# Performance work log

Hardware: AMD Instinct MI355X
Metric: run time of the kernel (lower is better)

The kernel has to match this reference:

```python
import jax, jax.numpy as jnp
import numpy as np

N, C, H, W = 64, 160, 64, 64
DIM, M = 160, 6
N_ITERS = 2
EPS_LN = 1e-5


def layer_norm(x, g, b):
    mu = jnp.mean(x, axis=-1, keepdims=True)
    var = jnp.var(x, axis=-1, keepdims=True)
    return (x - mu) * jax.lax.rsqrt(var + EPS_LN) * g + b


def setup_inputs() -> dict:
    key = jax.random.key(0)
    ks = jax.random.split(key, 10)
    d = DIM
    lin = lambda k, i, o: jax.random.normal(k, (i, o), jnp.float32) * (1.0 / np.sqrt(i))
    return {
        "feat": jax.random.normal(ks[0], (N, C, H, W), jnp.float32),
        "slots_init": jax.random.normal(ks[1], (M, d), jnp.float32) * 0.02,
        "log_tau": jnp.zeros((1,), jnp.float32),
        "kv_g": jnp.ones((C,), jnp.float32), "kv_b": jnp.zeros((C,), jnp.float32),
        "Wk": lin(ks[2], C, d), "Wv": lin(ks[3], C, d),
        "q_g": jnp.ones((d,), jnp.float32), "q_b": jnp.zeros((d,), jnp.float32),
        "Wq": lin(ks[4], d, d),
        "out_g": jnp.ones((d,), jnp.float32), "out_b": jnp.zeros((d,), jnp.float32),
        "W1": lin(ks[5], d, 2 * d), "b1": jnp.zeros((2 * d,), jnp.float32),
        "W2": lin(ks[6], 2 * d, d), "b2": jnp.zeros((d,), jnp.float32),
    }


def reference(feat, slots_init, log_tau, kv_g, kv_b, Wk, Wv, q_g, q_b, Wq,
              out_g, out_b, W1, b1, W2, b2):
    n, c, h, w = feat.shape
    scale = DIM ** (-0.5)
    # [n, l, c] tokens
    kv_in = layer_norm(feat.reshape(n, c, h * w).transpose(0, 2, 1), kv_g, kv_b)
    k = kv_in @ Wk  # [n, l, d]
    v = kv_in @ Wv  # [n, l, d]
    slots = jnp.broadcast_to(slots_init[None], (n, M, DIM))
    tau = jax.nn.softplus(log_tau) + 0.5  # [1]
    attn = None
    for _ in range(N_ITERS):
        q = layer_norm(slots, q_g, q_b) @ Wq  # [n, m, d]
        logits = jnp.einsum('nmd,nld->nml', q, k) * (scale / tau)
        attn = jax.nn.softmax(logits, axis=1)  # compete over slots
        weights = attn / jnp.clip(attn.sum(axis=-1, keepdims=True), 1e-6)
        updates = jnp.einsum('nml,nld->nmd', weights, v)
        slots = layer_norm(slots + updates, out_g, out_b)
        slots = slots + (jax.nn.gelu(slots @ W1 + b1, approximate=False) @ W2 + b2)
    attn_map = (attn / jnp.clip(attn.sum(axis=-1, keepdims=True), 1e-6)).reshape(n, M, h, w)
    return slots, attn_map
```

## Files before the change

### kernel.cpp

```cpp
#include <hip/hip_runtime.h>
#include <math.h>

#define NN 64
#define CC 160
#define LL 4096
#define DD 160
#define MM 6
#define NCH 16
#define NT 4
#define XSTR 68

#if defined(__has_builtin)
#if __has_builtin(__builtin_amdgcn_fdot2_f32_bf16)
#define HAVE_DOT2 1
#endif
#endif

__device__ __forceinline__ unsigned short f2bf(float f) {
  union { float f; unsigned int i; } v; v.f = f;
  unsigned int r = v.i + 0x7fffu + ((v.i >> 16) & 1u);
  return (unsigned short)(r >> 16);
}
__device__ __forceinline__ float u2f_lo(unsigned int w) {
  union { unsigned int i; float f; } v; v.i = w << 16; return v.f;
}
__device__ __forceinline__ float u2f_hi(unsigned int w) {
  union { unsigned int i; float f; } v; v.i = w & 0xffff0000u; return v.f;
}

#if HAVE_DOT2
typedef __bf16 v2bf __attribute__((ext_vector_type(2)));
__device__ __forceinline__ float dot2bf(unsigned int a, unsigned int b, float c) {
  union { unsigned int u; v2bf v; } ua, ub;
  ua.u = a; ub.u = b;
  return __builtin_amdgcn_fdot2_f32_bf16(ua.v, ub.v, c, false);
}
#else
__device__ __forceinline__ float dot2bf(unsigned int a, unsigned int b, float c) {
  return fmaf(u2f_hi(a), u2f_hi(b), fmaf(u2f_lo(a), u2f_lo(b), c));
}
#endif

__global__ __launch_bounds__(256) void k_trans(
    const float* __restrict__ Wv, const float* __restrict__ Wq,
    const float* __restrict__ W1, const float* __restrict__ W2,
    float* __restrict__ WvT, float* __restrict__ WqT,
    float* __restrict__ W1T, float* __restrict__ W2T) {
  int b = blockIdx.x;
  const float* src; float* dst; int R, C, tr, tc;
  if (b < 25)       { src = Wv; dst = WvT; R = 160; C = 160; int t = b;       tr = t / 5;  tc = t % 5; }
  else if (b < 50)  { src = Wq; dst = WqT; R = 160; C = 160; int t = b - 25;  tr = t / 5;  tc = t % 5; }
  else if (b < 100) { src = W1; dst = W1T; R = 160; C = 320; int t = b - 50;  tr = t / 10; tc = t % 10; }
  else              { src = W2; dst = W2T; R = 320; C = 160; int t = b - 100; tr = t / 5;  tc = t % 5; }
  __shared__ float tile[32][33];
  int r0 = tr * 32, c0 = tc * 32;
  int lr = threadIdx.x >> 5, lc = threadIdx.x & 31;
#pragma unroll
  for (int i = 0; i < 4; i++)
    tile[lr + i * 8][lc] = src[(size_t)(r0 + lr + i * 8) * C + c0 + lc];
  __syncthreads();
#pragma unroll
  for (int i = 0; i < 4; i++)
    dst[(size_t)(c0 + lr + i * 8) * R + r0 + lc] = tile[lc][lr + i * 8];
}

__global__ __launch_bounds__(512) void k_init(
    const float* log_tau, const float* slots_init, const float* q_g, const float* q_b,
    const float* Wq, const float* Wk, float* Wkq1, float* scal) {
  __shared__ float ln[MM * DD];
  __shared__ float qv[MM * DD];
  __shared__ float mu_s[MM], rs_s[MM];
  int bi = blockIdx.x, tid = threadIdx.x;
  float x = log_tau[0];
  float sp = (x > 20.f) ? x : log1pf(expf(x));
  float scv = (1.0f / sqrtf((float)DD)) / (sp + 0.5f);
  if (bi == 0 && tid == 0) scal[0] = scv;
  int w = tid >> 6, l = tid & 63;
  if (w < MM) {
    float x0 = slots_init[w * DD + l];
    float x1 = slots_init[w * DD + l + 64];
    float x2 = (l < 32) ? slots_init[w * DD + l + 128] : 0.f;
    float s = x0 + x1 + x2, ss = x0 * x0 + x1 * x1 + x2 * x2;
#pragma unroll
    for (int off = 32; off >= 1; off >>= 1) { s += __shfl_xor(s, off); ss += __shfl_xor(ss, off); }
    if (l == 0) {
      float mu = s / DD, var = ss / DD - mu * mu;
      mu_s[w] = mu; rs_s[w] = rsqrtf(var + 1e-5f);
    }
  }
  __syncthreads();
  for (int o = tid; o < MM * DD; o += 512) {
    int m = o / DD, d = o % DD;
    ln[o] = (slots_init[o] - mu_s[m]) * rs_s[m] * q_g[d] + q_b[d];
  }
  __syncthreads();
  for (int o = tid; o < MM * DD; o += 512) {
    int m = o / DD, d = o % DD;
    float acc = 0.f;
#pragma unroll 8
    for (int i = 0; i < DD; i++) acc = fmaf(ln[m * DD + i], Wq[i * DD + d], acc);
    qv[o] = acc;
  }
  __syncthreads();
  int grp = tid >> 4, l4 = tid & 15;
#pragma unroll
  for (int t = grp; t < 60; t += 32) {
    int c = bi * 10 + t / 6, m = t % 6;
    float s = 0.f;
#pragma unroll
    for (int i = 0; i < 10; i++) {
      int d = l4 + i * 16;
      s = fmaf(Wk[c * DD + d], qv[m * DD + d], s);
    }
    s += __shfl_xor(s, 1); s += __shfl_xor(s, 2);
    s += __shfl_xor(s, 4); s += __shfl_xor(s, 8);
    if (l4 == 0) Wkq1[c * 6 + m] = scv * s;
  }
}

__global__ __launch_bounds__(256) void k_init2(
    const float* Wkq1, const float* kv_g, const float* kv_b, float* P1, float* ab) {
  int tid = threadIdx.x;
  for (int o = tid; o < DD * 6; o += 256) {
    int c = o / 6;
    P1[o] = kv_g[c] * Wkq1[o];
  }
  if (tid < 192) {
    int grp = tid >> 4;
    int l = tid & 15;
    int m = grp % 6;
    const float* coef = (grp < 6) ? kv_g : kv_b;
    float s = 0.f;
#pragma unroll
    for (int i = 0; i < 10; i++) {
      int c = l + i * 16;
      s += coef[c] * Wkq1[c * 6 + m];
    }
    s += __shfl_xor(s, 1); s += __shfl_xor(s, 2);
    s += __shfl_xor(s, 4); s += __shfl_xor(s, 8);
    if (l == 0) ab[grp] = s;
  }
}

struct TileShared {
  unsigned short xb[160 * XSTR];
  float part[4][16][4][10];
  unsigned int w2_s[32][8];
  float P_s[160][8];
};

template <bool ITER2>
__device__ __forceinline__ void tile_body(
    TileShared* sh, const float* __restrict__ fb, const float* alpha, const float* beta,
    int tid, int lane, int g, int cg, int tl,
    float* Aacc, float* Sacc,
    float* __restrict__ attn_out, size_t attn_base) {
  float s4[4] = {0, 0, 0, 0}, ss4[4] = {0, 0, 0, 0};
  float lgr[6][4];
#pragma unroll
  for (int m = 0; m < 6; m++) { lgr[m][0] = 0.f; lgr[m][1] = 0.f; lgr[m][2] = 0.f; lgr[m][3] = 0.f; }
#pragma unroll
  for (int r = 0; r < 10; r++) {
    int c = g * 40 + r * 4 + cg;
    float4 xv = *(const float4*)(fb + (size_t)(r * 4) * LL);
    float4 p03 = *(const float4*)&sh->P_s[c][0];
    float2 p45 = *(const float2*)&sh->P_s[c][4];
    float xs[4] = {xv.x, xv.y, xv.z, xv.w};
#pragma unroll
    for (int j = 0; j < 4; j++) {
      float x = xs[j];
      s4[j] += x; ss4[j] = fmaf(x, x, ss4[j]);
      lgr[0][j] = fmaf(x, p03.x, lgr[0][j]); lgr[1][j] = fmaf(x, p03.y, lgr[1][j]);
      lgr[2][j] = fmaf(x, p03.z, lgr[2][j]); lgr[3][j] = fmaf(x, p03.w, lgr[3][j]);
      lgr[4][j] = fmaf(x, p45.x, lgr[4][j]); lgr[5][j] = fmaf(x, p45.y, lgr[5][j]);
    }
    uint2 pk;
    pk.x = (unsigned int)f2bf(xv.x) | ((unsigned int)f2bf(xv.y) << 16);
    pk.y = (unsigned int)f2bf(xv.z) | ((unsigned int)f2bf(xv.w) << 16);
    *(uint2*)&sh->xb[c * XSTR + 4 * tl] = pk;
  }
#pragma unroll
  for (int j = 0; j < 4; j++) {
    s4[j] += __shfl_xor(s4[j], 16);  s4[j] += __shfl_xor(s4[j], 32);
    ss4[j] += __shfl_xor(ss4[j], 16); ss4[j] += __shfl_xor(ss4[j], 32);
#pragma unroll
    for (int m = 0; m < 6; m++) {
      lgr[m][j] += __shfl_xor(lgr[m][j], 16);
      lgr[m][j] += __shfl_xor(lgr[m][j], 32);
    }
  }
  if (cg == 0) {
#pragma unroll
    for (int j = 0; j < 4; j++) {
      float* pp = &sh->part[g][tl][j][0];
      *(float2*)&pp[0] = make_float2(s4[j], ss4[j]);
      *(float2*)&pp[2] = make_float2(lgr[0][j], lgr[1][j]);
      *(float2*)&pp[4] = make_float2(lgr[2][j], lgr[3][j]);
      *(float2*)&pp[6] = make_float2(lgr[4][j], lgr[5][j]);
    }
  }
  __syncthreads();
  {
    int tg = lane >> 2, tj = lane & 3;
    float S = 0.f, SS = 0.f, L[6] = {0, 0, 0, 0, 0, 0};
#pragma unroll
    for (int g2 = 0; g2 < 4; g2++) {
      const float* pp = &sh->part[g2][tg][tj][0];
      float2 a = *(const float2*)&pp[0];
      float2 b2_ = *(const float2*)&pp[2];
      float2 c2 = *(const float2*)&pp[4];
      float2 d2 = *(const float2*)&pp[6];
      S += a.x; SS += a.y;
      L[0] += b2_.x; L[1] += b2_.y; L[2] += c2.x; L[3] += c2.y; L[4] += d2.x; L[5] += d2.y;
    }
    float mu = S * (1.0f / CC);
    float var = SS * (1.0f / CC) - mu * mu;
    float rs = rsqrtf(var + 1e-5f);
    float lg[6];
#pragma unroll
    for (int m = 0; m < 6; m++) lg[m] = rs * L[m] - rs * mu * alpha[m] + beta[m];
    float mx = lg[0];
#pragma unroll
    for (int m = 1; m < 6; m++) mx = fmaxf(mx, lg[m]);
    float e[6], sum = 0.f;
#pragma unroll
    for (int m = 0; m < 6; m++) { e[m] = __expf(lg[m] - mx); sum += e[m]; }
    float inv = 1.0f / sum;
    float att[6], wv[6];
#pragma unroll
    for (int m = 0; m < 6; m++) { att[m] = e[m] * inv; wv[m] = att[m] * rs; }
    if (g == 0) {
      float wo[6];
#pragma unroll
      for (int m = 0; m < 6; m++) wo[m] = __shfl_xor(wv[m], 1);
      if (!(lane & 1)) {
        int tp = lane >> 1;
        unsigned int pk[6];
#pragma unroll
        for (int m = 0; m < 6; m++) pk[m] = (unsigned int)f2bf(wv[m]) | ((unsigned int)f2bf(wo[m]) << 16);
        *(uint4*)&sh->w2_s[tp][0] = make_uint4(pk[0], pk[1], pk[2], pk[3]);
        *(uint2*)&sh->w2_s[tp][4] = make_uint2(pk[4], pk[5]);
      }
    } else if (g == 1) {
      if (ITER2) {
#pragma unroll
        for (int m = 0; m < 6; m++) attn_out[attn_base + lane + (size_t)m * LL] = att[m];
      }
    } else if (g == 2) {
#pragma unroll
      for (int m = 0; m < 6; m++) Sacc[m] += att[m];
    } else {
#pragma unroll
      for (int m = 0; m < 6; m++) Sacc[m] += wv[m] * mu;
    }
  }
  __syncthreads();
  if (tid < DD) {
    const unsigned short* xr = &sh->xb[tid * XSTR];
#pragma unroll
    for (int k = 0; k < 16; k++) {
      uint2 xw = *(const uint2*)(xr + 4 * k);
      uint4 wa0 = *(const uint4*)&sh->w2_s[2 * k][0];
      uint2 wb0 = *(const uint2*)&sh->w2_s[2 * k][4];
      uint4 wa1 = *(const uint4*)&sh->w2_s[2 * k + 1][0];
      uint2 wb1 = *(const uint2*)&sh->w2_s[2 * k + 1][4];
      Aacc[0] = dot2bf(wa0.x, xw.x, Aacc[0]); Aacc[1] = dot2bf(wa0.y, xw.x, Aacc[1]);
      Aacc[2] = dot2bf(wa0.z, xw.x, Aacc[2]); Aacc[3] = dot2bf(wa0.w, xw.x, Aacc[3]);
      Aacc[4] = dot2bf(wb0.x, xw.x, Aacc[4]); Aacc[5] = dot2bf(wb0.y, xw.x, Aacc[5]);
      Aacc[0] = dot2bf(wa1.x, xw.y, Aacc[0]); Aacc[1] = dot2bf(wa1.y, xw.y, Aacc[1]);
      Aacc[2] = dot2bf(wa1.z, xw.y, Aacc[2]); Aacc[3] = dot2bf(wa1.w, xw.y, Aacc[3]);
      Aacc[4] = dot2bf(wb1.x, xw.y, Aacc[4]); Aacc[5] = dot2bf(wb1.y, xw.y, Aacc[5]);
    }
  }
  __syncthreads();
}

template <bool ITER2>
__global__ __launch_bounds__(256) void k_pass(
    const float* __restrict__ feat, const float* __restrict__ Pg,
    const float* __restrict__ abg, float* __restrict__ Apart,
    float* __restrict__ SWpart, float* __restrict__ attn_out) {
  int b = blockIdx.x;
  int n = b >> 4, ch = b & 15;
  int tid = threadIdx.x;
  int lane = tid & 63, g = tid >> 6;
  int cg = lane >> 4, tl = lane & 15;
  __shared__ TileShared sh;

  const float* wsrc = ITER2 ? (Pg + (size_t)n * DD * 6) : Pg;
  for (int o = tid; o < DD * 6; o += 256) sh.P_s[o / 6][o % 6] = wsrc[o];
  const float* absrc = ITER2 ? (abg + n * 12) : abg;
  float alpha[6], beta[6];
#pragma unroll
  for (int m = 0; m < 6; m++) { alpha[m] = absrc[m]; beta[m] = absrc[6 + m]; }
  float Aacc[6] = {0, 0, 0, 0, 0, 0};
  float Sacc[6] = {0, 0, 0, 0, 0, 0};
  __syncthreads();

  const float* fb0 = feat + ((size_t)(n * CC + g * 40 + cg)) * LL + ch * (64 * NT) + 4 * tl;
#pragma unroll 1
  for (int t4 = 0; t4 < NT; t4++) {
    size_t ab_ = ((size_t)(n * MM)) * LL + ch * (64 * NT) + t4 * 64;
    tile_body<ITER2>(&sh, fb0 + t4 * 64, alpha, beta, tid, lane, g, cg, tl, Aacc, Sacc, attn_out, ab_);
  }
  if (g == 2 || g == 3) {
#pragma unroll
    for (int m = 0; m < 6; m++) {
      float v = Sacc[m];
      v += __shfl_xor(v, 1);  v += __shfl_xor(v, 2);  v += __shfl_xor(v, 4);
      v += __shfl_xor(v, 8);  v += __shfl_xor(v, 16); v += __shfl_xor(v, 32);
      if (lane == 0) SWpart[b * 12 + (g - 2) * 6 + m] = v;
    }
  }
  if (tid < DD) {
#pragma unroll
    for (int m = 0; m < 6; m++) Apart[((size_t)b * 6 + m) * DD + tid] = Aacc[m];
  }
}

template <bool FIRST, bool LAST>
__global__ __launch_bounds__(256) void k_slot4(
    const float* __restrict__ slots_init, const float* __restrict__ Apart,
    const float* __restrict__ SWpart,
    const float* __restrict__ WvT, const float* __restrict__ WqT,
    const float* __restrict__ W1T, const float* __restrict__ W2T,
    const float* __restrict__ out_g, const float* __restrict__ out_b,
    const float* __restrict__ b1, const float* __restrict__ b2,
    const float* __restrict__ q_g, const float* __restrict__ q_b,
    const float* __restrict__ Wk,
    const float* __restrict__ kv_g, const float* __restrict__ kv_b,
    const float* __restrict__ scal,
    float* __restrict__ slotbuf, float* __restrict__ P2, float* __restrict__ ab2,
    float* __restrict__ Sfin, float* __restrict__ out_slots) {
  int b = blockIdx.x;
  int n = b / MM, m = b % MM;
  int tid = threadIdx.x;
  __shared__ float a_s[DD];
  __shared__ float s1[DD];
  __shared__ float h[320];
  __shared__ float pg[DD], pb[DD];
  __shared__ float sw_s[2];
  __shared__ float Sv_s, mu_s, rs_s;

  if (tid < 32) {
    int p = tid & 15, which = tid >> 4;
    float v = SWpart[(size_t)(n * NCH + p) * 12 + m + 6 * which];
    v += __shfl_xor(v, 1); v += __shfl_xor(v, 2);
    v += __shfl_xor(v, 4); v += __shfl_xor(v, 8);
    if (p == 0) {
      sw_s[which] = v;
      if (which == 0) {
        float sc = fmaxf(v, 1e-6f);
        Sv_s = sc;
        if (LAST) Sfin[n * 6 + m] = sc;
      }
    }
  }
  __syncthreads();
  if (tid < DD) {
    const float* src = Apart + ((size_t)(n * NCH) * 6 + m) * DD + tid;
    float ar = 0.f;
#pragma unroll
    for (int p = 0; p < NCH; p++) ar += src[(size_t)p * 6 * DD];
    a_s[tid] = kv_g[tid] * (ar - sw_s[1]) + kv_b[tid] * sw_s[0];
  }
  __syncthreads();
  if (tid < DD) {
    const float4* wr = (const float4*)(WvT + (size_t)tid * DD);
    float u = 0.f;
#pragma unroll 8
    for (int c4 = 0; c4 < 40; c4++) {
      float4 w = wr[c4];
      const float* ap = &a_s[c4 * 4];
      u = fmaf(w.x, ap[0], u); u = fmaf(w.y, ap[1], u);
      u = fmaf(w.z, ap[2], u); u = fmaf(w.w, ap[3], u);
    }
    float prev = FIRST ? slots_init[m * DD + tid] : slotbuf[(size_t)n * MM * DD + m * DD + tid];
    s1[tid] = prev + u / Sv_s;
  }
  __syncthreads();
  if (tid < 64) {
    float x0 = s1[tid], x1 = s1[tid + 64], x2 = (tid < 32) ? s1[tid + 128] : 0.f;
    float s = x0 + x1 + x2, ss = x0 * x0 + x1 * x1 + x2 * x2;
#pragma unroll
    for (int off = 32; off >= 1; off >>= 1) { s += __shfl_xor(s, off); ss += __shfl_xor(ss, off); }
    if (tid == 0) {
      float mu = s / DD, var = ss / DD - mu * mu;
      mu_s = mu; rs_s = rsqrtf(var + 1e-5f);
    }
  }
  __syncthreads();
  if (tid < DD) s1[tid] = (s1[tid] - mu_s) * rs_s * out_g[tid] + out_b[tid];
  __syncthreads();
  for (int j = tid; j < 320; j += 256) {
    const float4* wr = (const float4*)(W1T + (size_t)j * DD);
    float acc = b1[j];
#pragma unroll 8
    for (int d4 = 0; d4 < 40; d4++) {
      float4 w = wr[d4];
      const float* sp = &s1[d4 * 4];
      acc = fmaf(w.x, sp[0], acc); acc = fmaf(w.y, sp[1], acc);
      acc = fmaf(w.z, sp[2], acc); acc = fmaf(w.w, sp[3], acc);
    }
    h[j] = 0.5f * acc * (1.0f + erff(acc * 0.70710678118f));
  }
  __syncthreads();
  if (tid < DD) {
    const float4* wr = (const float4*)(W2T + (size_t)tid * 320);
    float acc = b2[tid];
#pragma unroll 8
    for (int j4 = 0; j4 < 80; j4++) {
      float4 w = wr[j4];
      const float* hp = &h[j4 * 4];
      acc = fmaf(w.x, hp[0], acc); acc = fmaf(w.y, hp[1], acc);
      acc = fmaf(w.z, hp[2], acc); acc = fmaf(w.w, hp[3], acc);
    }
    float val = s1[tid] + acc;
    a_s[tid] = val;
    if (LAST) out_slots[(size_t)n * MM * DD + m * DD + tid] = val;
    else slotbuf[(size_t)n * MM * DD + m * DD + tid] = val;
  }
  if (!LAST) {
    __syncthreads();
    if (tid < 64) {
      float x0 = a_s[tid], x1 = a_s[tid + 64], x2 = (tid < 32) ? a_s[tid + 128] : 0.f;
      float s = x0 + x1 + x2, ss = x0 * x0 + x1 * x1 + x2 * x2;
#pragma unroll
      for (int off = 32; off >= 1; off >>= 1) { s += __shfl_xor(s, off); ss += __shfl_xor(ss, off); }
      if (tid == 0) {
        float mu = s / DD, var = ss / DD - mu * mu;
        mu_s = mu; rs_s = rsqrtf(var + 1e-5f);
      }
    }
    __syncthreads();
    if (tid < DD) s1[tid] = (a_s[tid] - mu_s) * rs_s * q_g[tid] + q_b[tid];
    __syncthreads();
    if (tid < DD) {
      const float4* wr = (const float4*)(WqT + (size_t)tid * DD);
      float acc = 0.f;
#pragma unroll 8
      for (int i4 = 0; i4 < 40; i4++) {
        float4 w = wr[i4];
        const float* sp = &s1[i4 * 4];
        acc = fmaf(w.x, sp[0], acc); acc = fmaf(w.y, sp[1], acc);
        acc = fmaf(w.z, sp[2], acc); acc = fmaf(w.w, sp[3], acc);
      }
      h[tid] = acc;
    }
    __syncthreads();
    if (tid < DD) {
      const float4* wr = (const float4*)(Wk + (size_t)tid * DD);
      float s = 0.f;
#pragma unroll 8
      for (int d4 = 0; d4 < 40; d4++) {
        float4 w = wr[d4];
        const float* hp = &h[d4 * 4];
        s = fmaf(w.x, hp[0], s); s = fmaf(w.y, hp[1], s);
        s = fmaf(w.z, hp[2], s); s = fmaf(w.w, hp[3], s);
      }
      float wrv = scal[0] * s;
      float gv = kv_g[tid] * wrv;
      P2[(size_t)n * DD * 6 + tid * 6 + m] = gv;
      pg[tid] = gv;
      pb[tid] = kv_b[tid] * wrv;
    }
    __syncthreads();
    if (tid < 128) {
      int w = tid >> 6, l = tid & 63;
      const float* src = (w == 0) ? pg : pb;
      float x0 = src[l], x1 = src[l + 64], x2 = (l < 32) ? src[l + 128] : 0.f;
      float s = x0 + x1 + x2;
#pragma unroll
      for (int off = 32; off >= 1; off >>= 1) s += __shfl_xor(s, off);
      if (l == 0) ab2[n * 12 + 6 * w + m] = s;
    }
  }
}

__global__ __launch_bounds__(256) void k_norm(float* attn, const float* Sfin) {
  int idx = blockIdx.x * 256 + threadIdx.x;
  size_t base = (size_t)idx * 4;
  int nm = (int)(base >> 12);
  float s = Sfin[nm];
  float4 v = *(float4*)(attn + base);
  float inv = 1.0f / s;
  v.x *= inv; v.y *= inv; v.z *= inv; v.w *= inv;
  *(float4*)(attn + base) = v;
}

extern "C" void kernel_launch(void* const* d_in, const int* in_sizes, int n_in,
                              void* d_out, int out_size, void* d_ws, size_t ws_size,
                              hipStream_t stream) {
  const float* feat       = (const float*)d_in[0];
  const float* slots_init = (const float*)d_in[1];
  const float* log_tau    = (const float*)d_in[2];
  const float* kv_g       = (const float*)d_in[3];
  const float* kv_b       = (const float*)d_in[4];
  const float* Wk         = (const float*)d_in[5];
  const float* Wv         = (const float*)d_in[6];
  const float* q_g        = (const float*)d_in[7];
  const float* q_b        = (const float*)d_in[8];
  const float* Wq         = (const float*)d_in[9];
  const float* out_g      = (const float*)d_in[10];
  const float* out_b      = (const float*)d_in[11];
  const float* W1         = (const float*)d_in[12];
  const float* b1         = (const float*)d_in[13];
  const float* W2         = (const float*)d_in[14];
  const float* b2         = (const float*)d_in[15];
  float* out = (float*)d_out;
  float* out_attn = out + NN * MM * DD;

  float* Wkq1   = (float*)d_ws;
  float* ab     = Wkq1 + DD * 6;
  float* P1     = ab + 16;
  float* P2     = P1 + DD * 6;
  float* ab2    = P2 + (size_t)NN * DD * 6;
  float* Apart  = ab2 + NN * 12;
  float* SWpart = Apart + (size_t)NN * NCH * MM * DD;
  float* Sfin   = SWpart + (size_t)NN * NCH * 12;
  float* scal   = Sfin + NN * MM;
  float* slotbuf = scal + 8;
  float* WvT    = slotbuf + NN * MM * DD;
  float* WqT    = WvT + DD * DD;
  float* W1T    = WqT + DD * DD;
  float* W2T    = W1T + DD * 320;
  size_t required = (size_t)((char*)(W2T + DD * 320) - (char*)d_ws);
  if (ws_size < required) return;

  k_trans<<<150, 256, 0, stream>>>(Wv, Wq, W1, W2, WvT, WqT, W1T, W2T);
  k_init<<<16, 512, 0, stream>>>(log_tau, slots_init, q_g, q_b, Wq, Wk, Wkq1, scal);
  k_init2<<<1, 256, 0, stream>>>(Wkq1, kv_g, kv_b, P1, ab);
  k_pass<false><<<NN * NCH, 256, 0, stream>>>(feat, P1, ab, Apart, SWpart, out_attn);
  k_slot4<true, false><<<NN * MM, 256, 0, stream>>>(slots_init, Apart, SWpart, WvT, WqT, W1T, W2T,
                                                    out_g, out_b, b1, b2, q_g, q_b, Wk, kv_g, kv_b,
                                                    scal, slotbuf, P2, ab2, Sfin, out);
  k_pass<true><<<NN * NCH, 256, 0, stream>>>(feat, P2, ab2, Apart, SWpart, out_attn);
  k_slot4<false, true><<<NN * MM, 256, 0, stream>>>(slots_init, Apart, SWpart, WvT, WqT, W1T, W2T,
                                                    out_g, out_b, b1, b2, q_g, q_b, Wk, kv_g, kv_b,
                                                    scal, slotbuf, P2, ab2, Sfin, out);
  k_norm<<<(NN * MM * LL) / 1024, 256, 0, stream>>>(out_attn, Sfin);
}
```

Before: 210.1 us.

## Merge setup kernels, fold attention normalization into final slot kernel, batch feature loads

Three small setup kernels (weight transposes, Wkq projection, P1/ab reduction) are merged into a single launch, with one extra block doing all the init work. The separate k_norm pass over the attention map is removed; the final slot kernel now rescales its own attention row in place. In k_pass the tile body is inlined and feature loads are issued in batches of five float4 to raise memory-level parallelism. The cost is more register pressure in k_pass and the whole init chain serialized in one block.

```diff
diff --git a/kernel.cpp b/kernel.cpp
--- a/kernel.cpp
+++ b/kernel.cpp
@@ -41,40 +41,44 @@
 }
 #endif
 
-__global__ __launch_bounds__(256) void k_trans(
+__global__ __launch_bounds__(512) void k_setup(
     const float* __restrict__ Wv, const float* __restrict__ Wq,
     const float* __restrict__ W1, const float* __restrict__ W2,
+    const float* __restrict__ log_tau, const float* __restrict__ slots_init,
+    const float* __restrict__ q_g, const float* __restrict__ q_b,
+    const float* __restrict__ Wk, const float* __restrict__ kv_g, const float* __restrict__ kv_b,
     float* __restrict__ WvT, float* __restrict__ WqT,
-    float* __restrict__ W1T, float* __restrict__ W2T) {
+    float* __restrict__ W1T, float* __restrict__ W2T,
+    float* __restrict__ P1, float* __restrict__ ab, float* __restrict__ scal) {
   int b = blockIdx.x;
-  const float* src; float* dst; int R, C, tr, tc;
-  if (b < 25)       { src = Wv; dst = WvT; R = 160; C = 160; int t = b;       tr = t / 5;  tc = t % 5; }
-  else if (b < 50)  { src = Wq; dst = WqT; R = 160; C = 160; int t = b - 25;  tr = t / 5;  tc = t % 5; }
-  else if (b < 100) { src = W1; dst = W1T; R = 160; C = 320; int t = b - 50;  tr = t / 10; tc = t % 10; }
-  else              { src = W2; dst = W2T; R = 320; C = 160; int t = b - 100; tr = t / 5;  tc = t % 5; }
-  __shared__ float tile[32][33];
-  int r0 = tr * 32, c0 = tc * 32;
-  int lr = threadIdx.x >> 5, lc = threadIdx.x & 31;
-#pragma unroll
-  for (int i = 0; i < 4; i++)
-    tile[lr + i * 8][lc] = src[(size_t)(r0 + lr + i * 8) * C + c0 + lc];
-  __syncthreads();
-#pragma unroll
-  for (int i = 0; i < 4; i++)
-    dst[(size_t)(c0 + lr + i * 8) * R + r0 + lc] = tile[lc][lr + i * 8];
-}
-
-__global__ __launch_bounds__(512) void k_init(
-    const float* log_tau, const float* slots_init, const float* q_g, const float* q_b,
-    const float* Wq, const float* Wk, float* Wkq1, float* scal) {
+  int tid = threadIdx.x;
+  if (b < 150) {
+    const float* src; float* dst; int R, C, tr, tc;
+    if (b < 25)       { src = Wv; dst = WvT; R = 160; C = 160; int t = b;       tr = t / 5;  tc = t % 5; }
+    else if (b < 50)  { src = Wq; dst = WqT; R = 160; C = 160; int t = b - 25;  tr = t / 5;  tc = t % 5; }
+    else if (b < 100) { src = W1; dst = W1T; R = 160; C = 320; int t = b - 50;  tr = t / 10; tc = t % 10; }
+    else              { src = W2; dst = W2T; R = 320; C = 160; int t = b - 100; tr = t / 5;  tc = t % 5; }
+    __shared__ float tile[32][33];
+    int r0 = tr * 32, c0 = tc * 32;
+    int lr = tid >> 5, lc = tid & 31;
+#pragma unroll
+    for (int i = 0; i < 2; i++)
+      tile[lr + i * 16][lc] = src[(size_t)(r0 + lr + i * 16) * C + c0 + lc];
+    __syncthreads();
+#pragma unroll
+    for (int i = 0; i < 2; i++)
+      dst[(size_t)(c0 + lr + i * 16) * R + r0 + lc] = tile[lc][lr + i * 16];
+    return;
+  }
   __shared__ float ln[MM * DD];
   __shared__ float qv[MM * DD];
+  __shared__ float pgb[MM * DD];
+  __shared__ float pbb[MM * DD];
   __shared__ float mu_s[MM], rs_s[MM];
-  int bi = blockIdx.x, tid = threadIdx.x;
   float x = log_tau[0];
   float sp = (x > 20.f) ? x : log1pf(expf(x));
   float scv = (1.0f / sqrtf((float)DD)) / (sp + 0.5f);
-  if (bi == 0 && tid == 0) scal[0] = scv;
+  if (tid == 0) scal[0] = scv;
   int w = tid >> 6, l = tid & 63;
   if (w < MM) {
     float x0 = slots_init[w * DD + l];
@@ -102,43 +106,35 @@
     qv[o] = acc;
   }
   __syncthreads();
-  int grp = tid >> 4, l4 = tid & 15;
-#pragma unroll
-  for (int t = grp; t < 60; t += 32) {
-    int c = bi * 10 + t / 6, m = t % 6;
+  for (int o = tid; o < MM * DD; o += 512) {
+    int c = o / 6, m = o % 6;
+    const float4* wr = (const float4*)(Wk + (size_t)c * DD);
+    const float* qm = &qv[m * DD];
     float s = 0.f;
-#pragma unroll
-    for (int i = 0; i < 10; i++) {
-      int d = l4 + i * 16;
-      s = fmaf(Wk[c * DD + d], qv[m * DD + d], s);
-    }
-    s += __shfl_xor(s, 1); s += __shfl_xor(s, 2);
-    s += __shfl_xor(s, 4); s += __shfl_xor(s, 8);
-    if (l4 == 0) Wkq1[c * 6 + m] = scv * s;
-  }
-}
-
-__global__ __launch_bounds__(256) void k_init2(
-    const float* Wkq1, const float* kv_g, const float* kv_b, float* P1, float* ab) {
-  int tid = threadIdx.x;
-  for (int o = tid; o < DD * 6; o += 256) {
-    int c = o / 6;
-    P1[o] = kv_g[c] * Wkq1[o];
-  }
-  if (tid < 192) {
-    int grp = tid >> 4;
-    int l = tid & 15;
+#pragma unroll 8
+    for (int d4 = 0; d4 < 40; d4++) {
+      float4 wv4 = wr[d4];
+      s = fmaf(wv4.x, qm[d4 * 4], s);     s = fmaf(wv4.y, qm[d4 * 4 + 1], s);
+      s = fmaf(wv4.z, qm[d4 * 4 + 2], s); s = fmaf(wv4.w, qm[d4 * 4 + 3], s);
+    }
+    float wrv = scv * s;
+    float gv = kv_g[c] * wrv;
+    P1[o] = gv;
+    pgb[o] = gv;
+    pbb[o] = kv_b[c] * wrv;
+  }
+  __syncthreads();
+  if (tid < 384) {
+    int grp = tid >> 5;
+    int l5 = tid & 31;
     int m = grp % 6;
-    const float* coef = (grp < 6) ? kv_g : kv_b;
+    const float* src = (grp < 6) ? pgb : pbb;
     float s = 0.f;
 #pragma unroll
-    for (int i = 0; i < 10; i++) {
-      int c = l + i * 16;
-      s += coef[c] * Wkq1[c * 6 + m];
-    }
-    s += __shfl_xor(s, 1); s += __shfl_xor(s, 2);
-    s += __shfl_xor(s, 4); s += __shfl_xor(s, 8);
-    if (l == 0) ab[grp] = s;
+    for (int i = 0; i < 5; i++) s += src[(l5 + i * 32) * 6 + m];
+    s += __shfl_xor(s, 1); s += __shfl_xor(s, 2); s += __shfl_xor(s, 4);
+    s += __shfl_xor(s, 8); s += __shfl_xor(s, 16);
+    if (l5 == 0) ab[grp] = s;
   }
 }
 
@@ -148,132 +144,6 @@
   unsigned int w2_s[32][8];
   float P_s[160][8];
 };
-
-template <bool ITER2>
-__device__ __forceinline__ void tile_body(
-    TileShared* sh, const float* __restrict__ fb, const float* alpha, const float* beta,
-    int tid, int lane, int g, int cg, int tl,
-    float* Aacc, float* Sacc,
-    float* __restrict__ attn_out, size_t attn_base) {
-  float s4[4] = {0, 0, 0, 0}, ss4[4] = {0, 0, 0, 0};
-  float lgr[6][4];
-#pragma unroll
-  for (int m = 0; m < 6; m++) { lgr[m][0] = 0.f; lgr[m][1] = 0.f; lgr[m][2] = 0.f; lgr[m][3] = 0.f; }
-#pragma unroll
-  for (int r = 0; r < 10; r++) {
-    int c = g * 40 + r * 4 + cg;
-    float4 xv = *(const float4*)(fb + (size_t)(r * 4) * LL);
-    float4 p03 = *(const float4*)&sh->P_s[c][0];
-    float2 p45 = *(const float2*)&sh->P_s[c][4];
-    float xs[4] = {xv.x, xv.y, xv.z, xv.w};
-#pragma unroll
-    for (int j = 0; j < 4; j++) {
-      float x = xs[j];
-      s4[j] += x; ss4[j] = fmaf(x, x, ss4[j]);
-      lgr[0][j] = fmaf(x, p03.x, lgr[0][j]); lgr[1][j] = fmaf(x, p03.y, lgr[1][j]);
-      lgr[2][j] = fmaf(x, p03.z, lgr[2][j]); lgr[3][j] = fmaf(x, p03.w, lgr[3][j]);
-      lgr[4][j] = fmaf(x, p45.x, lgr[4][j]); lgr[5][j] = fmaf(x, p45.y, lgr[5][j]);
-    }
-    uint2 pk;
-    pk.x = (unsigned int)f2bf(xv.x) | ((unsigned int)f2bf(xv.y) << 16);
-    pk.y = (unsigned int)f2bf(xv.z) | ((unsigned int)f2bf(xv.w) << 16);
-    *(uint2*)&sh->xb[c * XSTR + 4 * tl] = pk;
-  }
-#pragma unroll
-  for (int j = 0; j < 4; j++) {
-    s4[j] += __shfl_xor(s4[j], 16);  s4[j] += __shfl_xor(s4[j], 32);
-    ss4[j] += __shfl_xor(ss4[j], 16); ss4[j] += __shfl_xor(ss4[j], 32);
-#pragma unroll
-    for (int m = 0; m < 6; m++) {
-      lgr[m][j] += __shfl_xor(lgr[m][j], 16);
-      lgr[m][j] += __shfl_xor(lgr[m][j], 32);
-    }
-  }
-  if (cg == 0) {
-#pragma unroll
-    for (int j = 0; j < 4; j++) {
-      float* pp = &sh->part[g][tl][j][0];
-      *(float2*)&pp[0] = make_float2(s4[j], ss4[j]);
-      *(float2*)&pp[2] = make_float2(lgr[0][j], lgr[1][j]);
-      *(float2*)&pp[4] = make_float2(lgr[2][j], lgr[3][j]);
-      *(float2*)&pp[6] = make_float2(lgr[4][j], lgr[5][j]);
-    }
-  }
-  __syncthreads();
-  {
-    int tg = lane >> 2, tj = lane & 3;
-    float S = 0.f, SS = 0.f, L[6] = {0, 0, 0, 0, 0, 0};
-#pragma unroll
-    for (int g2 = 0; g2 < 4; g2++) {
-      const float* pp = &sh->part[g2][tg][tj][0];
-      float2 a = *(const float2*)&pp[0];
-      float2 b2_ = *(const float2*)&pp[2];
-      float2 c2 = *(const float2*)&pp[4];
-      float2 d2 = *(const float2*)&pp[6];
-      S += a.x; SS += a.y;
-      L[0] += b2_.x; L[1] += b2_.y; L[2] += c2.x; L[3] += c2.y; L[4] += d2.x; L[5] += d2.y;
-    }
-    float mu = S * (1.0f / CC);
-    float var = SS * (1.0f / CC) - mu * mu;
-    float rs = rsqrtf(var + 1e-5f);
-    float lg[6];
-#pragma unroll
-    for (int m = 0; m < 6; m++) lg[m] = rs * L[m] - rs * mu * alpha[m] + beta[m];
-    float mx = lg[0];
-#pragma unroll
-    for (int m = 1; m < 6; m++) mx = fmaxf(mx, lg[m]);
-    float e[6], sum = 0.f;
-#pragma unroll
-    for (int m = 0; m < 6; m++) { e[m] = __expf(lg[m] - mx); sum += e[m]; }
-    float inv = 1.0f / sum;
-    float att[6], wv[6];
-#pragma unroll
-    for (int m = 0; m < 6; m++) { att[m] = e[m] * inv; wv[m] = att[m] * rs; }
-    if (g == 0) {
-      float wo[6];
-#pragma unroll
-      for (int m = 0; m < 6; m++) wo[m] = __shfl_xor(wv[m], 1);
-      if (!(lane & 1)) {
-        int tp = lane >> 1;
-        unsigned int pk[6];
-#pragma unroll
-        for (int m = 0; m < 6; m++) pk[m] = (unsigned int)f2bf(wv[m]) | ((unsigned int)f2bf(wo[m]) << 16);
-        *(uint4*)&sh->w2_s[tp][0] = make_uint4(pk[0], pk[1], pk[2], pk[3]);
-        *(uint2*)&sh->w2_s[tp][4] = make_uint2(pk[4], pk[5]);
-      }
-    } else if (g == 1) {
-      if (ITER2) {
-#pragma unroll
-        for (int m = 0; m < 6; m++) attn_out[attn_base + lane + (size_t)m * LL] = att[m];
-      }
-    } else if (g == 2) {
-#pragma unroll
-      for (int m = 0; m < 6; m++) Sacc[m] += att[m];
-    } else {
-#pragma unroll
-      for (int m = 0; m < 6; m++) Sacc[m] += wv[m] * mu;
-    }
-  }
-  __syncthreads();
-  if (tid < DD) {
-    const unsigned short* xr = &sh->xb[tid * XSTR];
-#pragma unroll
-    for (int k = 0; k < 16; k++) {
-      uint2 xw = *(const uint2*)(xr + 4 * k);
-      uint4 wa0 = *(const uint4*)&sh->w2_s[2 * k][0];
-      uint2 wb0 = *(const uint2*)&sh->w2_s[2 * k][4];
-      uint4 wa1 = *(const uint4*)&sh->w2_s[2 * k + 1][0];
-      uint2 wb1 = *(const uint2*)&sh->w2_s[2 * k + 1][4];
-      Aacc[0] = dot2bf(wa0.x, xw.x, Aacc[0]); Aacc[1] = dot2bf(wa0.y, xw.x, Aacc[1]);
-      Aacc[2] = dot2bf(wa0.z, xw.x, Aacc[2]); Aacc[3] = dot2bf(wa0.w, xw.x, Aacc[3]);
-      Aacc[4] = dot2bf(wb0.x, xw.x, Aacc[4]); Aacc[5] = dot2bf(wb0.y, xw.x, Aacc[5]);
-      Aacc[0] = dot2bf(wa1.x, xw.y, Aacc[0]); Aacc[1] = dot2bf(wa1.y, xw.y, Aacc[1]);
-      Aacc[2] = dot2bf(wa1.z, xw.y, Aacc[2]); Aacc[3] = dot2bf(wa1.w, xw.y, Aacc[3]);
-      Aacc[4] = dot2bf(wb1.x, xw.y, Aacc[4]); Aacc[5] = dot2bf(wb1.y, xw.y, Aacc[5]);
-    }
-  }
-  __syncthreads();
-}
 
 template <bool ITER2>
 __global__ __launch_bounds__(256) void k_pass(
@@ -298,11 +168,138 @@
   __syncthreads();
 
   const float* fb0 = feat + ((size_t)(n * CC + g * 40 + cg)) * LL + ch * (64 * NT) + 4 * tl;
+
 #pragma unroll 1
   for (int t4 = 0; t4 < NT; t4++) {
-    size_t ab_ = ((size_t)(n * MM)) * LL + ch * (64 * NT) + t4 * 64;
-    tile_body<ITER2>(&sh, fb0 + t4 * 64, alpha, beta, tid, lane, g, cg, tl, Aacc, Sacc, attn_out, ab_);
-  }
+    const float* fb = fb0 + t4 * 64;
+    float s4[4] = {0, 0, 0, 0}, ss4[4] = {0, 0, 0, 0};
+    float lgr[6][4];
+#pragma unroll
+    for (int m = 0; m < 6; m++) { lgr[m][0] = 0.f; lgr[m][1] = 0.f; lgr[m][2] = 0.f; lgr[m][3] = 0.f; }
+#pragma unroll
+    for (int h5 = 0; h5 < 2; h5++) {
+      float4 xv[5];
+#pragma unroll
+      for (int r5 = 0; r5 < 5; r5++)
+        xv[r5] = *(const float4*)(fb + (size_t)((h5 * 5 + r5) * 4) * LL);
+#pragma unroll
+      for (int r5 = 0; r5 < 5; r5++) {
+        int r = h5 * 5 + r5;
+        int c = g * 40 + r * 4 + cg;
+        float4 p03 = *(const float4*)&sh.P_s[c][0];
+        float2 p45 = *(const float2*)&sh.P_s[c][4];
+        float xs[4] = {xv[r5].x, xv[r5].y, xv[r5].z, xv[r5].w};
+#pragma unroll
+        for (int j = 0; j < 4; j++) {
+          float xx = xs[j];
+          s4[j] += xx; ss4[j] = fmaf(xx, xx, ss4[j]);
+          lgr[0][j] = fmaf(xx, p03.x, lgr[0][j]); lgr[1][j] = fmaf(xx, p03.y, lgr[1][j]);
+          lgr[2][j] = fmaf(xx, p03.z, lgr[2][j]); lgr[3][j] = fmaf(xx, p03.w, lgr[3][j]);
+          lgr[4][j] = fmaf(xx, p45.x, lgr[4][j]); lgr[5][j] = fmaf(xx, p45.y, lgr[5][j]);
+        }
+        uint2 pk;
+        pk.x = (unsigned int)f2bf(xv[r5].x) | ((unsigned int)f2bf(xv[r5].y) << 16);
+        pk.y = (unsigned int)f2bf(xv[r5].z) | ((unsigned int)f2bf(xv[r5].w) << 16);
+        *(uint2*)&sh.xb[c * XSTR + 4 * tl] = pk;
+      }
+    }
+#pragma unroll
+    for (int j = 0; j < 4; j++) {
+      s4[j] += __shfl_xor(s4[j], 16);  s4[j] += __shfl_xor(s4[j], 32);
+      ss4[j] += __shfl_xor(ss4[j], 16); ss4[j] += __shfl_xor(ss4[j], 32);
+#pragma unroll
+      for (int m = 0; m < 6; m++) {
+        lgr[m][j] += __shfl_xor(lgr[m][j], 16);
+        lgr[m][j] += __shfl_xor(lgr[m][j], 32);
+      }
+    }
+    if (cg == 0) {
+#pragma unroll
+      for (int j = 0; j < 4; j++) {
+        float* pp = &sh.part[g][tl][j][0];
+        *(float2*)&pp[0] = make_float2(s4[j], ss4[j]);
+        *(float2*)&pp[2] = make_float2(lgr[0][j], lgr[1][j]);
+        *(float2*)&pp[4] = make_float2(lgr[2][j], lgr[3][j]);
+        *(float2*)&pp[6] = make_float2(lgr[4][j], lgr[5][j]);
+      }
+    }
+    __syncthreads();
+    {
+      int tg = lane >> 2, tj = lane & 3;
+      float S = 0.f, SS = 0.f, L[6] = {0, 0, 0, 0, 0, 0};
+#pragma unroll
+      for (int g2 = 0; g2 < 4; g2++) {
+        const float* pp = &sh.part[g2][tg][tj][0];
+        float2 a = *(const float2*)&pp[0];
+        float2 b2_ = *(const float2*)&pp[2];
+        float2 c2 = *(const float2*)&pp[4];
+        float2 d2 = *(const float2*)&pp[6];
+        S += a.x; SS += a.y;
+        L[0] += b2_.x; L[1] += b2_.y; L[2] += c2.x; L[3] += c2.y; L[4] += d2.x; L[5] += d2.y;
+      }
+      float mu = S * (1.0f / CC);
+      float var = SS * (1.0f / CC) - mu * mu;
+      float rs = rsqrtf(var + 1e-5f);
+      float lg[6];
+#pragma unroll
+      for (int m = 0; m < 6; m++) lg[m] = rs * L[m] - rs * mu * alpha[m] + beta[m];
+      float mx = lg[0];
+#pragma unroll
+      for (int m = 1; m < 6; m++) mx = fmaxf(mx, lg[m]);
+      float e[6], sum = 0.f;
+#pragma unroll
+      for (int m = 0; m < 6; m++) { e[m] = __expf(lg[m] - mx); sum += e[m]; }
+      float inv = 1.0f / sum;
+      float att[6], wv[6];
+#pragma unroll
+      for (int m = 0; m < 6; m++) { att[m] = e[m] * inv; wv[m] = att[m] * rs; }
+      if (g == 0) {
+        float wo[6];
+#pragma unroll
+        for (int m = 0; m < 6; m++) wo[m] = __shfl_xor(wv[m], 1);
+        if (!(lane & 1)) {
+          int tp = lane >> 1;
+          unsigned int pk[6];
+#pragma unroll
+          for (int m = 0; m < 6; m++) pk[m] = (unsigned int)f2bf(wv[m]) | ((unsigned int)f2bf(wo[m]) << 16);
+          *(uint4*)&sh.w2_s[tp][0] = make_uint4(pk[0], pk[1], pk[2], pk[3]);
+          *(uint2*)&sh.w2_s[tp][4] = make_uint2(pk[4], pk[5]);
+        }
+      } else if (g == 1) {
+        if (ITER2) {
+          size_t ob = ((size_t)(n * MM)) * LL + ch * (64 * NT) + t4 * 64 + lane;
+#pragma unroll
+          for (int m = 0; m < 6; m++) attn_out[ob + (size_t)m * LL] = att[m];
+        }
+      } else if (g == 2) {
+#pragma unroll
+        for (int m = 0; m < 6; m++) Sacc[m] += att[m];
+      } else {
+#pragma unroll
+        for (int m = 0; m < 6; m++) Sacc[m] += wv[m] * mu;
+      }
+    }
+    __syncthreads();
+    if (tid < DD) {
+      const unsigned short* xr = &sh.xb[tid * XSTR];
+#pragma unroll
+      for (int k = 0; k < 16; k++) {
+        uint2 xw = *(const uint2*)(xr + 4 * k);
+        uint4 wa0 = *(const uint4*)&sh.w2_s[2 * k][0];
+        uint2 wb0 = *(const uint2*)&sh.w2_s[2 * k][4];
+        uint4 wa1 = *(const uint4*)&sh.w2_s[2 * k + 1][0];
+        uint2 wb1 = *(const uint2*)&sh.w2_s[2 * k + 1][4];
+        Aacc[0] = dot2bf(wa0.x, xw.x, Aacc[0]); Aacc[1] = dot2bf(wa0.y, xw.x, Aacc[1]);
+        Aacc[2] = dot2bf(wa0.z, xw.x, Aacc[2]); Aacc[3] = dot2bf(wa0.w, xw.x, Aacc[3]);
+        Aacc[4] = dot2bf(wb0.x, xw.x, Aacc[4]); Aacc[5] = dot2bf(wb0.y, xw.x, Aacc[5]);
+        Aacc[0] = dot2bf(wa1.x, xw.y, Aacc[0]); Aacc[1] = dot2bf(wa1.y, xw.y, Aacc[1]);
+        Aacc[2] = dot2bf(wa1.z, xw.y, Aacc[2]); Aacc[3] = dot2bf(wa1.w, xw.y, Aacc[3]);
+        Aacc[4] = dot2bf(wb1.x, xw.y, Aacc[4]); Aacc[5] = dot2bf(wb1.y, xw.y, Aacc[5]);
+      }
+    }
+    __syncthreads();
+  }
+
   if (g == 2 || g == 3) {
 #pragma unroll
     for (int m = 0; m < 6; m++) {
@@ -331,7 +328,7 @@
     const float* __restrict__ kv_g, const float* __restrict__ kv_b,
     const float* __restrict__ scal,
     float* __restrict__ slotbuf, float* __restrict__ P2, float* __restrict__ ab2,
-    float* __restrict__ Sfin, float* __restrict__ out_slots) {
+    float* __restrict__ out_slots, float* __restrict__ attn) {
   int b = blockIdx.x;
   int n = b / MM, m = b % MM;
   int tid = threadIdx.x;
@@ -349,11 +346,7 @@
     v += __shfl_xor(v, 4); v += __shfl_xor(v, 8);
     if (p == 0) {
       sw_s[which] = v;
-      if (which == 0) {
-        float sc = fmaxf(v, 1e-6f);
-        Sv_s = sc;
-        if (LAST) Sfin[n * 6 + m] = sc;
-      }
+      if (which == 0) Sv_s = fmaxf(v, 1e-6f);
     }
   }
   __syncthreads();
@@ -420,7 +413,16 @@
     if (LAST) out_slots[(size_t)n * MM * DD + m * DD + tid] = val;
     else slotbuf[(size_t)n * MM * DD + m * DD + tid] = val;
   }
-  if (!LAST) {
+  if (LAST) {
+    float inv = 1.0f / Sv_s;
+    float4* arow = (float4*)(attn + ((size_t)(n * MM + m)) * LL);
+#pragma unroll
+    for (int i = tid; i < LL / 4; i += 256) {
+      float4 v = arow[i];
+      v.x *= inv; v.y *= inv; v.z *= inv; v.w *= inv;
+      arow[i] = v;
+    }
+  } else {
     __syncthreads();
     if (tid < 64) {
       float x0 = a_s[tid], x1 = a_s[tid + 64], x2 = (tid < 32) ? a_s[tid + 128] : 0.f;
@@ -475,17 +477,6 @@
       if (l == 0) ab2[n * 12 + 6 * w + m] = s;
     }
   }
-}
-
-__global__ __launch_bounds__(256) void k_norm(float* attn, const float* Sfin) {
-  int idx = blockIdx.x * 256 + threadIdx.x;
-  size_t base = (size_t)idx * 4;
-  int nm = (int)(base >> 12);
-  float s = Sfin[nm];
-  float4 v = *(float4*)(attn + base);
-  float inv = 1.0f / s;
-  v.x *= inv; v.y *= inv; v.z *= inv; v.w *= inv;
-  *(float4*)(attn + base) = v;
 }
 
 extern "C" void kernel_launch(void* const* d_in, const int* in_sizes, int n_in,
@@ -510,15 +501,13 @@
   float* out = (float*)d_out;
   float* out_attn = out + NN * MM * DD;
 
-  float* Wkq1   = (float*)d_ws;
-  float* ab     = Wkq1 + DD * 6;
+  float* ab     = (float*)d_ws;
   float* P1     = ab + 16;
   float* P2     = P1 + DD * 6;
   float* ab2    = P2 + (size_t)NN * DD * 6;
   float* Apart  = ab2 + NN * 12;
   float* SWpart = Apart + (size_t)NN * NCH * MM * DD;
-  float* Sfin   = SWpart + (size_t)NN * NCH * 12;
-  float* scal   = Sfin + NN * MM;
+  float* scal   = SWpart + (size_t)NN * NCH * 12;
   float* slotbuf = scal + 8;
   float* WvT    = slotbuf + NN * MM * DD;
   float* WqT    = WvT + DD * DD;
@@ -527,16 +516,14 @@
   size_t required = (size_t)((char*)(W2T + DD * 320) - (char*)d_ws);
   if (ws_size < required) return;
 
-  k_trans<<<150, 256, 0, stream>>>(Wv, Wq, W1, W2, WvT, WqT, W1T, W2T);
-  k_init<<<16, 512, 0, stream>>>(log_tau, slots_init, q_g, q_b, Wq, Wk, Wkq1, scal);
-  k_init2<<<1, 256, 0, stream>>>(Wkq1, kv_g, kv_b, P1, ab);
+  k_setup<<<151, 512, 0, stream>>>(Wv, Wq, W1, W2, log_tau, slots_init, q_g, q_b,
+                                   Wk, kv_g, kv_b, WvT, WqT, W1T, W2T, P1, ab, scal);
   k_pass<false><<<NN * NCH, 256, 0, stream>>>(feat, P1, ab, Apart, SWpart, out_attn);
   k_slot4<true, false><<<NN * MM, 256, 0, stream>>>(slots_init, Apart, SWpart, WvT, WqT, W1T, W2T,
                                                     out_g, out_b, b1, b2, q_g, q_b, Wk, kv_g, kv_b,
-                                                    scal, slotbuf, P2, ab2, Sfin, out);
+                                                    scal, slotbuf, P2, ab2, out, out_attn);
   k_pass<true><<<NN * NCH, 256, 0, stream>>>(feat, P2, ab2, Apart, SWpart, out_attn);
   k_slot4<false, true><<<NN * MM, 256, 0, stream>>>(slots_init, Apart, SWpart, WvT, WqT, W1T, W2T,
                                                     out_g, out_b, b1, b2, q_g, q_b, Wk, kv_g, kv_b,
-                                                    scal, slotbuf, P2, ab2, Sfin, out);
-  k_norm<<<(NN * MM * LL) / 1024, 256, 0, stream>>>(out_attn, Sfin);
-}
+                                                    scal, slotbuf, P2, ab2, out, out_attn);
+}
```

Result: no change. 206.8 us (-1.6%).
